# Performance work log

Measured on AMD Instinct MI355X. Metric: run time of the kernel, lower is better.

The kernel has to match this reference:

```python
import jax, jax.numpy as jnp
import numpy as np

B, V, H, T, D, HD = 4, 384, 128, 16, 8, 64
N = V + H  # 512
relu = jax.nn.relu


def setup_inputs() -> dict:
    key = jax.random.key(0)
    ks = jax.random.split(key, 12)

    def w(k, i, o):
        return (jax.random.normal(k, (i, o), jnp.float32) / np.sqrt(i)).astype(jnp.float32)

    return {
        "x": jax.random.normal(ks[0], (B, V, T, D), jnp.float32),
        "adj": jax.random.uniform(ks[1], (B, N, N), jnp.float32),
        # input_proj: Linear(T*D, HD) -> ReLU -> Linear(HD, HD) -> ReLU
        "w_in1": w(ks[2], T * D, HD), "b_in1": jnp.zeros((HD,), jnp.float32),
        "w_in2": w(ks[3], HD, HD), "b_in2": jnp.zeros((HD,), jnp.float32),
        # edge_mlp: Linear(2*HD, HD) -> ReLU -> Linear(HD, HD) -> ReLU
        "w_e1": w(ks[4], 2 * HD, HD), "b_e1": jnp.zeros((HD,), jnp.float32),
        "w_e2": w(ks[5], HD, HD), "b_e2": jnp.zeros((HD,), jnp.float32),
        # node_mlp: Linear(HD, HD) -> ReLU -> Linear(HD, HD) -> ReLU
        "w_n1": w(ks[6], HD, HD), "b_n1": jnp.zeros((HD,), jnp.float32),
        "w_n2": w(ks[7], HD, HD), "b_n2": jnp.zeros((HD,), jnp.float32),
        # out_proj: Linear(HD, T*D)
        "w_out": w(ks[8], HD, T * D), "b_out": jnp.zeros((T * D,), jnp.float32),
    }


def reference(x, adj, w_in1, b_in1, w_in2, b_in2, w_e1, b_e1, w_e2, b_e2,
              w_n1, b_n1, w_n2, b_n2, w_out, b_out):
    # node embedding of visible nodes: (B,V,HD)
    h = relu(relu(x.reshape(B, V, T * D) @ w_in1 + b_in1) @ w_in2 + b_in2)
    # pad hidden nodes with zeros: (B,N,HD)
    h_full = jnp.zeros((B, N, HD), x.dtype).at[:, :V].set(h)
    # edge_mlp layer 1 on cat([h_i, h_j]): split weight instead of materializing
    # the (B,N,N,2*HD) concatenation — same math.
    a = h_full @ w_e1[:HD]   # receiver-side contribution (B,N,HD)
    b = h_full @ w_e1[HD:]   # sender-side contribution  (B,N,HD)
    e = relu(a[:, :, None, :] + b[:, None, :, :] + b_e1)   # (B,N,N,HD)
    e = relu(e @ w_e2 + b_e2)                               # (B,N,N,HD)
    # mask by adjacency and sum over senders j
    agg = jnp.einsum('bijh,bij->bih', e, adj)               # (B,N,HD)
    n = relu(relu(agg @ w_n1 + b_n1) @ w_n2 + b_n2)         # (B,N,HD)
    out = n[:, V:] @ w_out + b_out                          # (B,H,T*D)
    return out.reshape(B, H, T, D)
```

## Files before the change

### kernel.cpp

```cpp
#include <hip/hip_runtime.h>

#define BQ 4
#define VV 384
#define HH 128
#define NN 512
#define HDIM 64
#define TD 128

__device__ __forceinline__ float BCAST(float v, int l) {
    return __int_as_float(__builtin_amdgcn_readlane(__float_as_int(v), l));
}

__global__ __launch_bounds__(64) void k_rowpipe(
    const float* __restrict__ x,
    const float* __restrict__ w_in1,
    const float* __restrict__ b_in1,
    const float* __restrict__ w_in2,
    const float* __restrict__ b_in2,
    const float* __restrict__ w_e1,
    const float* __restrict__ b_e1,
    const float* __restrict__ w_e2,
    const float* __restrict__ b_e2,
    float* __restrict__ E2)
{
    const int row  = blockIdx.x;
    const int lane = threadIdx.x;

    const float* xr = x + (size_t)row * TD;
    const float xv0 = xr[lane];
    const float xv1 = xr[64 + lane];

    float a0 = b_in1[lane], a1 = 0.f;
    #pragma unroll 8
    for (int k = 0; k < HDIM; ++k) {
        a0 = fmaf(BCAST(xv0, k), w_in1[k * HDIM + lane],          a0);
        a1 = fmaf(BCAST(xv1, k), w_in1[(HDIM + k) * HDIM + lane], a1);
    }
    const float h1 = fmaxf(a0 + a1, 0.f);

    a0 = b_in2[lane]; a1 = 0.f;
    #pragma unroll 8
    for (int k = 0; k < HDIM; k += 2) {
        a0 = fmaf(BCAST(h1, k),     w_in2[k * HDIM + lane],       a0);
        a1 = fmaf(BCAST(h1, k + 1), w_in2[(k + 1) * HDIM + lane], a1);
    }
    const float h2 = fmaxf(a0 + a1, 0.f);

    a0 = 0.f; a1 = 0.f;
    #pragma unroll 8
    for (int k = 0; k < HDIM; k += 2) {
        a0 = fmaf(BCAST(h2, k),     w_e1[(HDIM + k) * HDIM + lane],     a0);
        a1 = fmaf(BCAST(h2, k + 1), w_e1[(HDIM + k + 1) * HDIM + lane], a1);
    }
    const float e1 = fmaxf(a0 + a1 + b_e1[lane], 0.f);

    a0 = b_e2[lane]; a1 = 0.f;
    #pragma unroll 8
    for (int k = 0; k < HDIM; k += 2) {
        a0 = fmaf(BCAST(e1, k),     w_e2[k * HDIM + lane],       a0);
        a1 = fmaf(BCAST(e1, k + 1), w_e2[(k + 1) * HDIM + lane], a1);
    }
    E2[(size_t)row * HDIM + lane] = fmaxf(a0 + a1, 0.f);
}

__global__ __launch_bounds__(1024) void k_agg_out(
    const float* __restrict__ adj,
    const float* __restrict__ E2,
    const float* __restrict__ b_e1, const float* __restrict__ w_e2,
    const float* __restrict__ b_e2,
    const float* __restrict__ w_n1, const float* __restrict__ b_n1,
    const float* __restrict__ w_n2, const float* __restrict__ b_n2,
    const float* __restrict__ w_out,
    const float* __restrict__ b_out,
    float* __restrict__ out)
{
    const int blk  = blockIdx.x;
    const int b    = blk >> 6;
    const int pair = blk & 63;
    const int wid  = threadIdx.x >> 6;
    const int lane = threadIdx.x & 63;

    const int i0 = VV + pair * 2;
    const float* adjr0 = adj + ((size_t)b * NN + i0) * NN;
    const float* adjr1 = adjr0 + NN;
    const int j0 = wid * 32;

    const float adjv = (lane < 32) ? adjr0[j0 + lane] : adjr1[j0 + lane - 32];

    __shared__ float redA[12][2][HDIM];
    __shared__ float hs[4][2];
    __shared__ float e2c[HDIM];

    if (wid < 12) {
        const float* e2b = E2 + ((size_t)b * VV + j0) * HDIM;
        float p0 = 0.f, p1 = 0.f, q0 = 0.f, q1 = 0.f;
        #pragma unroll 8
        for (int jj = 0; jj < 32; jj += 2) {
            const float e0 = e2b[jj * HDIM + lane];
            const float e1 = e2b[(jj + 1) * HDIM + lane];
            p0 = fmaf(BCAST(adjv, jj),      e0, p0);
            q0 = fmaf(BCAST(adjv, 32 + jj), e0, q0);
            p1 = fmaf(BCAST(adjv, jj + 1),  e1, p1);
            q1 = fmaf(BCAST(adjv, 33 + jj), e1, q1);
        }
        redA[wid][0][lane] = p0 + p1;
        redA[wid][1][lane] = q0 + q1;
    } else {
        float s = adjv;
        s += __shfl_xor(s, 1, 64);
        s += __shfl_xor(s, 2, 64);
        s += __shfl_xor(s, 4, 64);
        s += __shfl_xor(s, 8, 64);
        s += __shfl_xor(s, 16, 64);
        if (lane == 0)  hs[wid - 12][0] = s;
        if (lane == 32) hs[wid - 12][1] = s;
        if (wid == 12) {
            const float e1c = fmaxf(b_e1[lane], 0.f);
            float t0 = b_e2[lane], t1 = 0.f;
            #pragma unroll 8
            for (int k = 0; k < HDIM; k += 2) {
                t0 = fmaf(BCAST(e1c, k),     w_e2[k * HDIM + lane],       t0);
                t1 = fmaf(BCAST(e1c, k + 1), w_e2[(k + 1) * HDIM + lane], t1);
            }
            e2c[lane] = fmaxf(t0 + t1, 0.f);
        }
    }
    __syncthreads();

    const int g  = wid >> 3;
    const int w8 = wid & 7;
    if (w8 >= 2) return;

    const float hsum = hs[0][g] + hs[1][g] + hs[2][g] + hs[3][g];
    float agg = hsum * e2c[lane];
    #pragma unroll
    for (int w = 0; w < 12; ++w) agg += redA[w][g][lane];

    float t0 = b_n1[lane], t1 = 0.f;
    #pragma unroll 8
    for (int k = 0; k < HDIM; k += 2) {
        t0 = fmaf(BCAST(agg, k),     w_n1[k * HDIM + lane],       t0);
        t1 = fmaf(BCAST(agg, k + 1), w_n1[(k + 1) * HDIM + lane], t1);
    }
    const float n1 = fmaxf(t0 + t1, 0.f);

    t0 = b_n2[lane]; t1 = 0.f;
    #pragma unroll 8
    for (int k = 0; k < HDIM; k += 2) {
        t0 = fmaf(BCAST(n1, k),     w_n2[k * HDIM + lane],       t0);
        t1 = fmaf(BCAST(n1, k + 1), w_n2[(k + 1) * HDIM + lane], t1);
    }
    const float n2 = fmaxf(t0 + t1, 0.f);

    const int col = 64 * w8 + lane;
    float o0 = b_out[col], o1 = 0.f;
    #pragma unroll 8
    for (int k = 0; k < HDIM; k += 2) {
        o0 = fmaf(BCAST(n2, k),     w_out[k * TD + col],       o0);
        o1 = fmaf(BCAST(n2, k + 1), w_out[(k + 1) * TD + col], o1);
    }
    const int orow = b * HH + pair * 2 + g;
    out[(size_t)orow * TD + col] = o0 + o1;
}

extern "C" void kernel_launch(void* const* d_in, const int* in_sizes, int n_in,
                              void* d_out, int out_size, void* d_ws, size_t ws_size,
                              hipStream_t stream) {
    const float* x     = (const float*)d_in[0];
    const float* adj   = (const float*)d_in[1];
    const float* w_in1 = (const float*)d_in[2];
    const float* b_in1 = (const float*)d_in[3];
    const float* w_in2 = (const float*)d_in[4];
    const float* b_in2 = (const float*)d_in[5];
    const float* w_e1  = (const float*)d_in[6];
    const float* b_e1  = (const float*)d_in[7];
    const float* w_e2  = (const float*)d_in[8];
    const float* b_e2  = (const float*)d_in[9];
    const float* w_n1  = (const float*)d_in[10];
    const float* b_n1  = (const float*)d_in[11];
    const float* w_n2  = (const float*)d_in[12];
    const float* b_n2  = (const float*)d_in[13];
    const float* w_out = (const float*)d_in[14];
    const float* b_out = (const float*)d_in[15];
    float* out = (float*)d_out;
    float* E2  = (float*)d_ws;

    k_rowpipe<<<BQ * VV, 64, 0, stream>>>(
        x, w_in1, b_in1, w_in2, b_in2, w_e1, b_e1, w_e2, b_e2, E2);
    k_agg_out<<<BQ * HH / 2, 1024, 0, stream>>>(
        adj, E2, b_e1, w_e2, b_e2, w_n1, b_n1, w_n2, b_n2, w_out, b_out, out);
}
```

Before: 19.14 us.

## Split row MLP K-dimension across two waves per row, six rows per block

The per-row MLP kernel now gives each row two wavefronts, and each one handles half of the reduction dimension for every layer. Partial sums are combined through shared memory with block-wide barriers. Six rows are packed into a 768-thread block, so there are 256 blocks instead of 1536 single-wave blocks. This halves the serial FMA/readlane chain per wave and improves latency hiding. The cost is four __syncthreads barriers, shared-memory traffic, and a grid of only 256 blocks on a GPU with many CUs.

```diff
diff --git a/kernel.cpp b/kernel.cpp
--- a/kernel.cpp
+++ b/kernel.cpp
@@ -11,7 +11,7 @@
     return __int_as_float(__builtin_amdgcn_readlane(__float_as_int(v), l));
 }
 
-__global__ __launch_bounds__(64) void k_rowpipe(
+__global__ __launch_bounds__(768) void k_rowpipe(
     const float* __restrict__ x,
     const float* __restrict__ w_in1,
     const float* __restrict__ b_in1,
@@ -23,44 +23,62 @@
     const float* __restrict__ b_e2,
     float* __restrict__ E2)
 {
-    const int row  = blockIdx.x;
-    const int lane = threadIdx.x;
+    __shared__ float part[4][6][2][HDIM];
+
+    const int wid  = threadIdx.x >> 6;
+    const int lane = threadIdx.x & 63;
+    const int rl   = wid >> 1;
+    const int hf   = wid & 1;
+    const int row  = blockIdx.x * 6 + rl;
 
     const float* xr = x + (size_t)row * TD;
-    const float xv0 = xr[lane];
-    const float xv1 = xr[64 + lane];
-
-    float a0 = b_in1[lane], a1 = 0.f;
-    #pragma unroll 8
-    for (int k = 0; k < HDIM; ++k) {
-        a0 = fmaf(BCAST(xv0, k), w_in1[k * HDIM + lane],          a0);
-        a1 = fmaf(BCAST(xv1, k), w_in1[(HDIM + k) * HDIM + lane], a1);
-    }
-    const float h1 = fmaxf(a0 + a1, 0.f);
-
-    a0 = b_in2[lane]; a1 = 0.f;
-    #pragma unroll 8
-    for (int k = 0; k < HDIM; k += 2) {
-        a0 = fmaf(BCAST(h1, k),     w_in2[k * HDIM + lane],       a0);
-        a1 = fmaf(BCAST(h1, k + 1), w_in2[(k + 1) * HDIM + lane], a1);
-    }
-    const float h2 = fmaxf(a0 + a1, 0.f);
+    const float xv = xr[64 * hf + lane];
+
+    float a0 = 0.f, a1 = 0.f;
+    #pragma unroll 8
+    for (int k = 0; k < 64; k += 2) {
+        const int kg = 64 * hf + k;
+        a0 = fmaf(BCAST(xv, k),     w_in1[kg * HDIM + lane],       a0);
+        a1 = fmaf(BCAST(xv, k + 1), w_in1[(kg + 1) * HDIM + lane], a1);
+    }
+    part[0][rl][hf][lane] = a0 + a1;
+    __syncthreads();
+    const float h1 = fmaxf(part[0][rl][0][lane] + part[0][rl][1][lane] + b_in1[lane], 0.f);
 
     a0 = 0.f; a1 = 0.f;
     #pragma unroll 8
-    for (int k = 0; k < HDIM; k += 2) {
-        a0 = fmaf(BCAST(h2, k),     w_e1[(HDIM + k) * HDIM + lane],     a0);
-        a1 = fmaf(BCAST(h2, k + 1), w_e1[(HDIM + k + 1) * HDIM + lane], a1);
-    }
-    const float e1 = fmaxf(a0 + a1 + b_e1[lane], 0.f);
-
-    a0 = b_e2[lane]; a1 = 0.f;
-    #pragma unroll 8
-    for (int k = 0; k < HDIM; k += 2) {
-        a0 = fmaf(BCAST(e1, k),     w_e2[k * HDIM + lane],       a0);
-        a1 = fmaf(BCAST(e1, k + 1), w_e2[(k + 1) * HDIM + lane], a1);
-    }
-    E2[(size_t)row * HDIM + lane] = fmaxf(a0 + a1, 0.f);
+    for (int k = 0; k < 32; k += 2) {
+        const int kg = 32 * hf + k;
+        a0 = fmaf(BCAST(h1, kg),     w_in2[kg * HDIM + lane],       a0);
+        a1 = fmaf(BCAST(h1, kg + 1), w_in2[(kg + 1) * HDIM + lane], a1);
+    }
+    part[1][rl][hf][lane] = a0 + a1;
+    __syncthreads();
+    const float h2 = fmaxf(part[1][rl][0][lane] + part[1][rl][1][lane] + b_in2[lane], 0.f);
+
+    a0 = 0.f; a1 = 0.f;
+    #pragma unroll 8
+    for (int k = 0; k < 32; k += 2) {
+        const int kg = 32 * hf + k;
+        a0 = fmaf(BCAST(h2, kg),     w_e1[(HDIM + kg) * HDIM + lane],     a0);
+        a1 = fmaf(BCAST(h2, kg + 1), w_e1[(HDIM + kg + 1) * HDIM + lane], a1);
+    }
+    part[2][rl][hf][lane] = a0 + a1;
+    __syncthreads();
+    const float e1 = fmaxf(part[2][rl][0][lane] + part[2][rl][1][lane] + b_e1[lane], 0.f);
+
+    a0 = 0.f; a1 = 0.f;
+    #pragma unroll 8
+    for (int k = 0; k < 32; k += 2) {
+        const int kg = 32 * hf + k;
+        a0 = fmaf(BCAST(e1, kg),     w_e2[kg * HDIM + lane],       a0);
+        a1 = fmaf(BCAST(e1, kg + 1), w_e2[(kg + 1) * HDIM + lane], a1);
+    }
+    part[3][rl][hf][lane] = a0 + a1;
+    __syncthreads();
+    if (hf == 0)
+        E2[(size_t)row * HDIM + lane] =
+            fmaxf(part[3][rl][0][lane] + part[3][rl][1][lane] + b_e2[lane], 0.f);
 }
 
 __global__ __launch_bounds__(1024) void k_agg_out(
@@ -185,7 +203,7 @@
     float* out = (float*)d_out;
     float* E2  = (float*)d_ws;
 
-    k_rowpipe<<<BQ * VV, 64, 0, stream>>>(
+    k_rowpipe<<<BQ * VV / 6, 768, 0, stream>>>(
         x, w_in1, b_in1, w_in2, b_in2, w_e1, b_e1, w_e2, b_e2, E2);
     k_agg_out<<<BQ * HH / 2, 1024, 0, stream>>>(
         adj, E2, b_e1, w_e2, b_e2, w_n1, b_n1, w_n2, b_n2, w_out, b_out, out);
```

After: 20.01 us. 4.6% more time.
